# Kernel optimization log

Measured on AMD Instinct MI355X. Metric: run time of the kernel, lower is better.

## Reference

```python
import jax, jax.numpy as jnp
import numpy as np

B, SQ, SK, H, NH = 2, 2048, 2048, 2048, 16
HD = H // NH  # 128
NEG = -1e9


def setup_inputs() -> dict:
    key = jax.random.key(0)
    ks = jax.random.split(key, 8)
    hidden_states = jax.random.normal(ks[0], (B, SQ, H), dtype=jnp.float32)
    # key already transposed/expanded for baddbmm: [B*nh, head_dim, key_len]
    k = jax.random.normal(ks[1], (B * NH, HD, SK), dtype=jnp.float32)
    v = jax.random.normal(ks[2], (B, NH, SK, HD), dtype=jnp.float32)
    # additive float causal mask [B, 1, Sq, Sk]
    causal = jnp.tril(jnp.ones((SQ, SK), dtype=bool))
    attention_mask = jnp.where(causal, 0.0, NEG).astype(jnp.float32)
    attention_mask = jnp.broadcast_to(attention_mask[None, None], (B, 1, SQ, SK))
    w_q = jax.random.normal(ks[3], (H, H), dtype=jnp.float32) * 0.02
    b_q = jnp.zeros((H,), dtype=jnp.float32)
    w_proj = jax.random.normal(ks[4], (H, H), dtype=jnp.float32) * 0.02
    b_proj = jnp.zeros((H,), dtype=jnp.float32)
    return {
        "hidden_states": hidden_states,
        "key": k,
        "value": v,
        "attention_mask": attention_mask,
        "w_q": w_q,
        "b_q": b_q,
        "w_proj": w_proj,
        "b_proj": b_proj,
    }


def reference(hidden_states, key, value, attention_mask, w_q, b_q, w_proj, b_proj):
    dtype = hidden_states.dtype
    scale = 1.0 / (HD ** 0.5)  # scale_attn_weights=True, attention_multiplier=None
    # q projection: [B, Sq, H] -> [B, nh, Sq, hd]
    q = hidden_states @ w_q.T + b_q
    q = q.reshape(B, SQ, NH, HD).transpose(0, 2, 1, 3)
    # key comes in as [B*nh, hd, Sk]
    k = key.reshape(B, NH, HD, SK)
    # scores = mask + scale * q @ k  (baddbmm with beta=1)
    scores = attention_mask + scale * jnp.einsum("bhqd,bhdk->bhqk", q, k)
    # softmax in fp32 (attention_softmax_in_fp32=True), cast back
    probs = jax.nn.softmax(scores.astype(jnp.float32), axis=-1).astype(dtype)
    # attn_pdrop=0 -> no dropout
    out = jnp.einsum("bhqk,bhkd->bhqd", probs, value)  # [B, nh, Sq, hd]
    out = out.transpose(0, 2, 1, 3).reshape(B, SQ, H)
    out = out @ w_proj.T + b_proj  # resid_pdrop=0 -> no dropout
    return out
```

## Files before the change

### kernel.cpp

```cpp
#include <hip/hip_runtime.h>
#include <hip/hip_bf16.h>

typedef __bf16 bf16;
typedef __bf16 bf16x4 __attribute__((ext_vector_type(4)));
typedef __bf16 bf16x8 __attribute__((ext_vector_type(8)));
typedef float  f32x4  __attribute__((ext_vector_type(4)));
typedef unsigned int u32;

#define B_   2
#define SQ_  2048
#define SK_  2048
#define H_   2048
#define NH_  16
#define HD_  128
#define BH_  (B_*NH_)

__device__ inline void gl_lds16(const bf16* g, bf16* l) {
  __builtin_amdgcn_global_load_lds(
      (const __attribute__((address_space(1))) u32*)(const void*)g,
      (__attribute__((address_space(3))) u32*)(void*)l,
      16, 0, 0);
}

__device__ inline float exp2_fast(float x) {
  float r; asm("v_exp_f32 %0, %1" : "=v"(r) : "v"(x)); return r;
}

__global__ __launch_bounds__(256) void cvt_f32_bf16(const float* __restrict__ in,
                                                    bf16* __restrict__ out, int n4) {
  int i = blockIdx.x * blockDim.x + threadIdx.x;
  int stride = gridDim.x * blockDim.x;
  for (; i < n4; i += stride) {
    float4 v = ((const float4*)in)[i];
    bf16x4 w; w[0] = (bf16)v.x; w[1] = (bf16)v.y; w[2] = (bf16)v.z; w[3] = (bf16)v.w;
    ((bf16x4*)out)[i] = w;
  }
}

__global__ __launch_bounds__(256) void transpose_cvt(const float* __restrict__ in,
                                                     bf16* __restrict__ out, int R, int C) {
  __shared__ float tile[64][65];
  const int bh = blockIdx.z;
  const int r0 = blockIdx.y * 64, c0 = blockIdx.x * 64;
  const float* src = in + (size_t)bh * R * C;
  bf16* dst = out + (size_t)bh * R * C;
  const int t = threadIdx.x;
  const int tx = t & 15, ty = t >> 4;
#pragma unroll
  for (int p = 0; p < 4; ++p) {
    int rr = ty + p * 16;
    float4 v = *(const float4*)&src[(size_t)(r0 + rr) * C + c0 + tx * 4];
    tile[rr][tx * 4 + 0] = v.x; tile[rr][tx * 4 + 1] = v.y;
    tile[rr][tx * 4 + 2] = v.z; tile[rr][tx * 4 + 3] = v.w;
  }
  __syncthreads();
#pragma unroll
  for (int p = 0; p < 4; ++p) {
    int cc = ty + p * 16;
    bf16x4 w;
#pragma unroll
    for (int i = 0; i < 4; ++i) w[i] = (bf16)tile[tx * 4 + i][cc];
    *(bf16x4*)&dst[(size_t)(c0 + cc) * R + r0 + tx * 4] = w;
  }
}

template <typename OutT>
__global__ __launch_bounds__(256) void gemm_bt(const bf16* __restrict__ A,
                                               const bf16* __restrict__ Bw,
                                               const float* __restrict__ bias,
                                               OutT* __restrict__ C,
                                               int M, int N, int K, float osc) {
  __shared__ bf16 Abuf[128 * 32];
  __shared__ bf16 Bbuf[128 * 32];
  const int nbn = N >> 7;
  int wg = blockIdx.x, nwg = gridDim.x;
  int swz = (nwg & 7) ? wg : ((wg & 7) * (nwg >> 3) + (wg >> 3));
  int bm = swz / nbn, bn = swz % nbn;
  const int t = threadIdx.x, lane = t & 63, wid = t >> 6;
  const int r = lane & 15, g = lane >> 4;
  const int wr = wid >> 1, wc = wid & 1;
  const size_t m0 = (size_t)bm * 128, n0 = (size_t)bn * 128;

  f32x4 acc[4][4];
#pragma unroll
  for (int m = 0; m < 4; ++m)
#pragma unroll
    for (int n = 0; n < 4; ++n) acc[m][n] = (f32x4){0.f, 0.f, 0.f, 0.f};

  for (int k0 = 0; k0 < K; k0 += 32) {
    __syncthreads();
#pragma unroll
    for (int p = 0; p < 2; ++p) {
      int c = p * 256 + t;
      int row = c >> 2, off = c & 3;
      gl_lds16(A + (m0 + row) * K + k0 + off * 8, &Abuf[(p * 256 + wid * 64) * 8]);
      gl_lds16(Bw + (n0 + row) * K + k0 + off * 8, &Bbuf[(p * 256 + wid * 64) * 8]);
    }
    __syncthreads();
    bf16x8 af[4], bfr[4];
#pragma unroll
    for (int m = 0; m < 4; ++m)
      af[m] = *(const bf16x8*)&Abuf[(wr * 64 + m * 16 + r) * 32 + g * 8];
#pragma unroll
    for (int n = 0; n < 4; ++n)
      bfr[n] = *(const bf16x8*)&Bbuf[(wc * 64 + n * 16 + r) * 32 + g * 8];
#pragma unroll
    for (int m = 0; m < 4; ++m)
#pragma unroll
      for (int n = 0; n < 4; ++n)
        acc[m][n] = __builtin_amdgcn_mfma_f32_16x16x32_bf16(af[m], bfr[n], acc[m][n], 0, 0, 0);
  }

  float bv[4];
#pragma unroll
  for (int n = 0; n < 4; ++n) bv[n] = bias[n0 + wc * 64 + n * 16 + r];
#pragma unroll
  for (int m = 0; m < 4; ++m)
#pragma unroll
    for (int n = 0; n < 4; ++n)
#pragma unroll
      for (int rr = 0; rr < 4; ++rr) {
        size_t row = m0 + wr * 64 + m * 16 + g * 4 + rr;
        size_t col = n0 + wc * 64 + n * 16 + r;
        C[row * N + col] = (OutT)((acc[m][n][rr] + bv[n]) * osc);
      }
}

__device__ __forceinline__ void softmax_prep(const f32x4 (&s)[4], bool diag,
                                             int r, int g, int qbase,
                                             float (&mrun)[4], float (&lpart)[4],
                                             f32x4 (&acc)[8], bf16* pldsw,
                                             bf16x8 (&pa)[2]) {
  float sv[4][4];
#pragma unroll
  for (int sb = 0; sb < 4; ++sb)
#pragma unroll
    for (int rr = 0; rr < 4; ++rr) {
      float x = s[sb][rr];
      if (diag && (sb * 16 + r > qbase + g * 4 + rr)) x = -3.0e38f;
      sv[sb][rr] = x;
    }
  float pm[4];
  bool cond = true;
#pragma unroll
  for (int rr = 0; rr < 4; ++rr) {
    pm[rr] = fmaxf(fmaxf(sv[0][rr], sv[1][rr]), fmaxf(sv[2][rr], sv[3][rr]));
    cond = cond && (pm[rr] <= mrun[rr] + 10.0f);
  }
  if (!__all(cond ? 1 : 0)) {
    f32x4 corrv;
#pragma unroll
    for (int rr = 0; rr < 4; ++rr) {
      float mx = pm[rr];
#pragma unroll
      for (int d = 1; d < 16; d <<= 1) mx = fmaxf(mx, __shfl_xor(mx, d));
      float mnew = fmaxf(mrun[rr], mx);
      float corr = exp2_fast(mrun[rr] - mnew);
      mrun[rr] = mnew;
      lpart[rr] *= corr;
      corrv[rr] = corr;
    }
#pragma unroll
    for (int nb = 0; nb < 8; ++nb) acc[nb] *= corrv;
  }
#pragma unroll
  for (int sb = 0; sb < 4; ++sb)
#pragma unroll
    for (int rr = 0; rr < 4; ++rr) {
      float p = exp2_fast(sv[sb][rr] - mrun[rr]);
      lpart[rr] += p;
      pldsw[(g * 4 + rr) * 68 + sb * 16 + r] = (bf16)p;
    }
#pragma unroll
  for (int k2 = 0; k2 < 2; ++k2)
    pa[k2] = *(const bf16x8*)&pldsw[r * 68 + k2 * 32 + g * 8];
}

__global__ __launch_bounds__(256, 2) void flash_attn(const bf16* __restrict__ Q,
                                                     const bf16* __restrict__ Kt,
                                                     const bf16* __restrict__ Vt,
                                                     bf16* __restrict__ O) {
  __shared__ bf16 Klds[2][64 * 128];
  __shared__ bf16 Vlds[2][128 * 64];
  __shared__ bf16 Plds[4][16 * 68];

  const int id = blockIdx.x;
  const int pr = (id >> 3) & 15;
  const int bh = (id & 7) + 8 * (id >> 7);
  const int qtA = 31 - pr, qtB = pr;
  const int b = bh >> 4, h = bh & 15;
  const int t = threadIdx.x, lane = t & 63, wid = t >> 6;
  const int r = lane & 15, g = lane >> 4;

  const bf16* Kbase = Kt + (size_t)bh * SK_ * HD_;
  const bf16* Vbase = Vt + (size_t)bh * HD_ * SK_;
  bf16* pldsw = &Plds[wid][0];

  size_t kSrc[4], vSrc[4];
#pragma unroll
  for (int p = 0; p < 4; ++p) {
    int c = p * 256 + t;
    { int row = c >> 4, off = c & 15, src = off ^ (row & 7);
      kSrc[p] = (size_t)row * HD_ + src * 8; }
    { int row = c >> 3, off = c & 7, src = off ^ (row & 7);
      vSrc[p] = (size_t)row * SK_ + src * 8; }
  }

  const size_t qrowA = ((size_t)(b * SQ_ + qtA * 64 + wid * 16 + r)) * H_ + (size_t)h * HD_;
  const size_t qrowB = ((size_t)(b * SQ_ + qtB * 64 + wid * 16 + r)) * H_ + (size_t)h * HD_;
  bf16x8 qfA[4], qfB[4];
#pragma unroll
  for (int kk = 0; kk < 4; ++kk) {
    qfA[kk] = *(const bf16x8*)&Q[qrowA + kk * 32 + g * 8];
    qfB[kk] = *(const bf16x8*)&Q[qrowB + kk * 32 + g * 8];
  }

  f32x4 accA[8], accB[8];
  float mrunA[4], lpartA[4], mrunB[4], lpartB[4];
#pragma unroll
  for (int i = 0; i < 8; ++i) { accA[i] = (f32x4){0.f,0.f,0.f,0.f}; accB[i] = (f32x4){0.f,0.f,0.f,0.f}; }
#pragma unroll
  for (int i = 0; i < 4; ++i) { mrunA[i] = -3.0e38f; lpartA[i] = 0.f; mrunB[i] = -3.0e38f; lpartB[i] = 0.f; }

  int cur = 0;
#pragma unroll
  for (int p = 0; p < 4; ++p) {
    gl_lds16(Kbase + kSrc[p], &Klds[cur][(p * 256 + wid * 64) * 8]);
    gl_lds16(Vbase + vSrc[p], &Vlds[cur][(p * 256 + wid * 64) * 8]);
  }
  asm volatile("s_waitcnt vmcnt(0)" ::: "memory");
  __syncthreads();

#pragma unroll 1
  for (int st = 0; st <= qtA; ++st) {
    if (st < qtA) {
      const size_t ks = (size_t)(st + 1) * 64 * HD_;
      const size_t vs = (size_t)(st + 1) * 64;
#pragma unroll
      for (int p = 0; p < 4; ++p) {
        gl_lds16(Kbase + ks + kSrc[p], &Klds[cur ^ 1][(p * 256 + wid * 64) * 8]);
        gl_lds16(Vbase + vs + vSrc[p], &Vlds[cur ^ 1][(p * 256 + wid * 64) * 8]);
      }
    }
    const bool both = (st <= qtB);

    f32x4 sA[4], sB[4];
#pragma unroll
    for (int sb = 0; sb < 4; ++sb) { sA[sb] = (f32x4){0.f,0.f,0.f,0.f}; sB[sb] = (f32x4){0.f,0.f,0.f,0.f}; }
    __builtin_amdgcn_s_setprio(1);
    if (both) {
#pragma unroll
      for (int sb = 0; sb < 4; ++sb) {
        const int srow = sb * 16 + r;
#pragma unroll
        for (int kk = 0; kk < 4; ++kk) {
          bf16x8 kf = *(const bf16x8*)&Klds[cur][srow * 128 + (((kk * 4 + g) ^ (srow & 7)) * 8)];
          sA[sb] = __builtin_amdgcn_mfma_f32_16x16x32_bf16(qfA[kk], kf, sA[sb], 0, 0, 0);
          sB[sb] = __builtin_amdgcn_mfma_f32_16x16x32_bf16(qfB[kk], kf, sB[sb], 0, 0, 0);
        }
      }
    } else {
#pragma unroll
      for (int sb = 0; sb < 4; ++sb) {
        const int srow = sb * 16 + r;
#pragma unroll
        for (int kk = 0; kk < 4; ++kk) {
          bf16x8 kf = *(const bf16x8*)&Klds[cur][srow * 128 + (((kk * 4 + g) ^ (srow & 7)) * 8)];
          sA[sb] = __builtin_amdgcn_mfma_f32_16x16x32_bf16(qfA[kk], kf, sA[sb], 0, 0, 0);
        }
      }
    }
    __builtin_amdgcn_s_setprio(0);

    bf16x8 paA[2], paB[2];
    softmax_prep(sA, st == qtA, r, g, wid * 16, mrunA, lpartA, accA, pldsw, paA);
    if (both) softmax_prep(sB, st == qtB, r, g, wid * 16, mrunB, lpartB, accB, pldsw, paB);

    __builtin_amdgcn_s_setprio(1);
    if (both) {
#pragma unroll
      for (int nb = 0; nb < 8; ++nb) {
        const int drow = nb * 16 + r;
#pragma unroll
        for (int k2 = 0; k2 < 2; ++k2) {
          bf16x8 vf = *(const bf16x8*)&Vlds[cur][drow * 64 + (((k2 * 4 + g) ^ (drow & 7)) * 8)];
          accA[nb] = __builtin_amdgcn_mfma_f32_16x16x32_bf16(paA[k2], vf, accA[nb], 0, 0, 0);
          accB[nb] = __builtin_amdgcn_mfma_f32_16x16x32_bf16(paB[k2], vf, accB[nb], 0, 0, 0);
        }
      }
    } else {
#pragma unroll
      for (int nb = 0; nb < 8; ++nb) {
        const int drow = nb * 16 + r;
#pragma unroll
        for (int k2 = 0; k2 < 2; ++k2) {
          bf16x8 vf = *(const bf16x8*)&Vlds[cur][drow * 64 + (((k2 * 4 + g) ^ (drow & 7)) * 8)];
          accA[nb] = __builtin_amdgcn_mfma_f32_16x16x32_bf16(paA[k2], vf, accA[nb], 0, 0, 0);
        }
      }
    }
    __builtin_amdgcn_s_setprio(0);

    asm volatile("s_waitcnt vmcnt(0)" ::: "memory");
    __syncthreads();
    cur ^= 1;
  }

  float invA[4], invB[4];
#pragma unroll
  for (int rr = 0; rr < 4; ++rr) {
    float la = lpartA[rr], lb = lpartB[rr];
#pragma unroll
    for (int d = 1; d < 16; d <<= 1) { la += __shfl_xor(la, d); lb += __shfl_xor(lb, d); }
    invA[rr] = 1.0f / la; invB[rr] = 1.0f / lb;
  }
#pragma unroll
  for (int nb = 0; nb < 8; ++nb)
#pragma unroll
    for (int rr = 0; rr < 4; ++rr) {
      size_t rowA = (size_t)(b * SQ_ + qtA * 64 + wid * 16 + g * 4 + rr);
      size_t rowB = (size_t)(b * SQ_ + qtB * 64 + wid * 16 + g * 4 + rr);
      O[rowA * H_ + (size_t)h * HD_ + nb * 16 + r] = (bf16)(accA[nb][rr] * invA[rr]);
      O[rowB * H_ + (size_t)h * HD_ + nb * 16 + r] = (bf16)(accB[nb][rr] * invB[rr]);
    }
}

extern "C" void kernel_launch(void* const* d_in, const int* in_sizes, int n_in,
                              void* d_out, int out_size, void* d_ws, size_t ws_size,
                              hipStream_t stream) {
  const float* hidden = (const float*)d_in[0];
  const float* key    = (const float*)d_in[1];
  const float* value  = (const float*)d_in[2];
  const float* w_q    = (const float*)d_in[4];
  const float* b_q    = (const float*)d_in[5];
  const float* w_proj = (const float*)d_in[6];
  const float* b_proj = (const float*)d_in[7];
  float* out = (float*)d_out;

  const size_t N_HID = (size_t)B_ * SQ_ * H_;
  const size_t N_W   = (size_t)H_ * H_;
  const size_t N_KV  = (size_t)BH_ * SK_ * HD_;
  const float SC2 = 0.08838834764831845f * 1.4426950408889634f;

  bf16* hid_bf  = (bf16*)d_ws;
  bf16* wq_bf   = hid_bf + N_HID;
  bf16* wp_bf   = wq_bf + N_W;
  bf16* k_bf    = wp_bf + N_W;
  bf16* vt_bf   = k_bf + N_KV;
  bf16* q_bf    = vt_bf + N_KV;
  bf16* attn_bf = hid_bf;

  cvt_f32_bf16<<<2048, 256, 0, stream>>>(hidden, hid_bf, (int)(N_HID / 4));
  cvt_f32_bf16<<<1024, 256, 0, stream>>>(w_q, wq_bf, (int)(N_W / 4));
  cvt_f32_bf16<<<1024, 256, 0, stream>>>(w_proj, wp_bf, (int)(N_W / 4));
  transpose_cvt<<<dim3(SK_ / 64, HD_ / 64, BH_), 256, 0, stream>>>(key, k_bf, HD_, SK_);
  transpose_cvt<<<dim3(HD_ / 64, SK_ / 64, BH_), 256, 0, stream>>>(value, vt_bf, SK_, HD_);

  gemm_bt<bf16><<<(B_ * SQ_ / 128) * (H_ / 128), 256, 0, stream>>>(
      hid_bf, wq_bf, b_q, q_bf, B_ * SQ_, H_, H_, SC2);

  flash_attn<<<512, 256, 0, stream>>>(q_bf, k_bf, vt_bf, attn_bf);

  gemm_bt<float><<<(B_ * SQ_ / 128) * (H_ / 128), 256, 0, stream>>>(
      attn_bf, wp_bf, b_proj, out, B_ * SQ_, H_, H_, 1.0f);
}
```

Before: 235.1 us.

## Use 128-row query tiles with two sequential passes per flash-attention block

Flash attention now assigns each block two 128-row query tiles (a far tile and a near tile), processed one after the other, with each wave owning 32 query rows as two 16-row fragments. Previously each block interleaved two 64-row tiles. The larger tile lets each K/V tile loaded into shared memory serve twice as many query rows, cutting K/V traffic. The grid halves to 256 blocks and launch bounds drop to one block per SM, which lowers occupancy and may leave CUs underused. Causal masking handles partially active fragments near the diagonal.

After: 249.0 us. 1.06x slower.

```diff
diff --git a/kernel.cpp b/kernel.cpp
--- a/kernel.cpp
+++ b/kernel.cpp
@@ -127,7 +127,7 @@
 }
 
 __device__ __forceinline__ void softmax_prep(const f32x4 (&s)[4], bool diag,
-                                             int r, int g, int qbase,
+                                             int r, int g, int qrow_base, int s_base,
                                              float (&mrun)[4], float (&lpart)[4],
                                              f32x4 (&acc)[8], bf16* pldsw,
                                              bf16x8 (&pa)[2]) {
@@ -137,7 +137,7 @@
 #pragma unroll
     for (int rr = 0; rr < 4; ++rr) {
       float x = s[sb][rr];
-      if (diag && (sb * 16 + r > qbase + g * 4 + rr)) x = -3.0e38f;
+      if (diag && (s_base + sb * 16 + r > qrow_base + g * 4 + rr)) x = -3.0e38f;
       sv[sb][rr] = x;
     }
   float pm[4];
@@ -176,25 +176,24 @@
     pa[k2] = *(const bf16x8*)&pldsw[r * 68 + k2 * 32 + g * 8];
 }
 
-__global__ __launch_bounds__(256, 2) void flash_attn(const bf16* __restrict__ Q,
+__global__ __launch_bounds__(256, 1) void flash_attn(const bf16* __restrict__ Q,
                                                      const bf16* __restrict__ Kt,
                                                      const bf16* __restrict__ Vt,
                                                      bf16* __restrict__ O) {
   __shared__ bf16 Klds[2][64 * 128];
   __shared__ bf16 Vlds[2][128 * 64];
-  __shared__ bf16 Plds[4][16 * 68];
+  __shared__ bf16 Plds[4][2][16 * 68];
 
   const int id = blockIdx.x;
-  const int pr = (id >> 3) & 15;
-  const int bh = (id & 7) + 8 * (id >> 7);
-  const int qtA = 31 - pr, qtB = pr;
+  const int pr = (id >> 3) & 7;
+  const int bh = (id & 7) + 8 * (id >> 6);
+  const int qtA = 15 - pr, qtB = pr;
   const int b = bh >> 4, h = bh & 15;
   const int t = threadIdx.x, lane = t & 63, wid = t >> 6;
   const int r = lane & 15, g = lane >> 4;
 
   const bf16* Kbase = Kt + (size_t)bh * SK_ * HD_;
   const bf16* Vbase = Vt + (size_t)bh * HD_ * SK_;
-  bf16* pldsw = &Plds[wid][0];
 
   size_t kSrc[4], vSrc[4];
 #pragma unroll
@@ -206,123 +205,143 @@
       vSrc[p] = (size_t)row * SK_ + src * 8; }
   }
 
-  const size_t qrowA = ((size_t)(b * SQ_ + qtA * 64 + wid * 16 + r)) * H_ + (size_t)h * HD_;
-  const size_t qrowB = ((size_t)(b * SQ_ + qtB * 64 + wid * 16 + r)) * H_ + (size_t)h * HD_;
-  bf16x8 qfA[4], qfB[4];
-#pragma unroll
-  for (int kk = 0; kk < 4; ++kk) {
-    qfA[kk] = *(const bf16x8*)&Q[qrowA + kk * 32 + g * 8];
-    qfB[kk] = *(const bf16x8*)&Q[qrowB + kk * 32 + g * 8];
-  }
-
-  f32x4 accA[8], accB[8];
-  float mrunA[4], lpartA[4], mrunB[4], lpartB[4];
-#pragma unroll
-  for (int i = 0; i < 8; ++i) { accA[i] = (f32x4){0.f,0.f,0.f,0.f}; accB[i] = (f32x4){0.f,0.f,0.f,0.f}; }
-#pragma unroll
-  for (int i = 0; i < 4; ++i) { mrunA[i] = -3.0e38f; lpartA[i] = 0.f; mrunB[i] = -3.0e38f; lpartB[i] = 0.f; }
-
   int cur = 0;
-#pragma unroll
-  for (int p = 0; p < 4; ++p) {
-    gl_lds16(Kbase + kSrc[p], &Klds[cur][(p * 256 + wid * 64) * 8]);
-    gl_lds16(Vbase + vSrc[p], &Vlds[cur][(p * 256 + wid * 64) * 8]);
-  }
-  asm volatile("s_waitcnt vmcnt(0)" ::: "memory");
-  __syncthreads();
-
 #pragma unroll 1
-  for (int st = 0; st <= qtA; ++st) {
-    if (st < qtA) {
-      const size_t ks = (size_t)(st + 1) * 64 * HD_;
-      const size_t vs = (size_t)(st + 1) * 64;
-#pragma unroll
-      for (int p = 0; p < 4; ++p) {
-        gl_lds16(Kbase + ks + kSrc[p], &Klds[cur ^ 1][(p * 256 + wid * 64) * 8]);
-        gl_lds16(Vbase + vs + vSrc[p], &Vlds[cur ^ 1][(p * 256 + wid * 64) * 8]);
-      }
-    }
-    const bool both = (st <= qtB);
-
-    f32x4 sA[4], sB[4];
-#pragma unroll
-    for (int sb = 0; sb < 4; ++sb) { sA[sb] = (f32x4){0.f,0.f,0.f,0.f}; sB[sb] = (f32x4){0.f,0.f,0.f,0.f}; }
-    __builtin_amdgcn_s_setprio(1);
-    if (both) {
-#pragma unroll
-      for (int sb = 0; sb < 4; ++sb) {
-        const int srow = sb * 16 + r;
-#pragma unroll
-        for (int kk = 0; kk < 4; ++kk) {
-          bf16x8 kf = *(const bf16x8*)&Klds[cur][srow * 128 + (((kk * 4 + g) ^ (srow & 7)) * 8)];
-          sA[sb] = __builtin_amdgcn_mfma_f32_16x16x32_bf16(qfA[kk], kf, sA[sb], 0, 0, 0);
-          sB[sb] = __builtin_amdgcn_mfma_f32_16x16x32_bf16(qfB[kk], kf, sB[sb], 0, 0, 0);
+  for (int pass = 0; pass < 2; ++pass) {
+    const int qt = pass ? qtB : qtA;
+    const int nst = 2 * qt + 2;
+    const int wb = qt * 128 + wid * 32;
+
+    bf16x8 qf[2][4];
+#pragma unroll
+    for (int m = 0; m < 2; ++m) {
+      const size_t qrow = ((size_t)(b * SQ_ + wb + m * 16 + r)) * H_ + (size_t)h * HD_;
+#pragma unroll
+      for (int kk = 0; kk < 4; ++kk)
+        qf[m][kk] = *(const bf16x8*)&Q[qrow + kk * 32 + g * 8];
+    }
+
+    f32x4 acc[2][8];
+    float mrun[2][4], lpart[2][4];
+#pragma unroll
+    for (int m = 0; m < 2; ++m) {
+#pragma unroll
+      for (int i = 0; i < 8; ++i) acc[m][i] = (f32x4){0.f, 0.f, 0.f, 0.f};
+#pragma unroll
+      for (int i = 0; i < 4; ++i) { mrun[m][i] = -3.0e38f; lpart[m][i] = 0.f; }
+    }
+
+#pragma unroll
+    for (int p = 0; p < 4; ++p) {
+      gl_lds16(Kbase + kSrc[p], &Klds[cur][(p * 256 + wid * 64) * 8]);
+      gl_lds16(Vbase + vSrc[p], &Vlds[cur][(p * 256 + wid * 64) * 8]);
+    }
+    asm volatile("s_waitcnt vmcnt(0)" ::: "memory");
+    __syncthreads();
+
+#pragma unroll 1
+    for (int st = 0; st < nst; ++st) {
+      if (st + 1 < nst) {
+        const size_t ks = (size_t)(st + 1) * 64 * HD_;
+        const size_t vs = (size_t)(st + 1) * 64;
+#pragma unroll
+        for (int p = 0; p < 4; ++p) {
+          gl_lds16(Kbase + ks + kSrc[p], &Klds[cur ^ 1][(p * 256 + wid * 64) * 8]);
+          gl_lds16(Vbase + vs + vSrc[p], &Vlds[cur ^ 1][(p * 256 + wid * 64) * 8]);
         }
       }
-    } else {
-#pragma unroll
-      for (int sb = 0; sb < 4; ++sb) {
-        const int srow = sb * 16 + r;
-#pragma unroll
-        for (int kk = 0; kk < 4; ++kk) {
-          bf16x8 kf = *(const bf16x8*)&Klds[cur][srow * 128 + (((kk * 4 + g) ^ (srow & 7)) * 8)];
-          sA[sb] = __builtin_amdgcn_mfma_f32_16x16x32_bf16(qfA[kk], kf, sA[sb], 0, 0, 0);
+      const int sb0 = st * 64;
+      const bool act1 = (sb0 <= wb + 31);
+      const bool act0 = (sb0 <= wb + 15);
+
+      if (act1) {
+        f32x4 sA[2][4];
+#pragma unroll
+        for (int m = 0; m < 2; ++m)
+#pragma unroll
+          for (int sb = 0; sb < 4; ++sb) sA[m][sb] = (f32x4){0.f, 0.f, 0.f, 0.f};
+        __builtin_amdgcn_s_setprio(1);
+        if (act0) {
+#pragma unroll
+          for (int sb = 0; sb < 4; ++sb) {
+            const int srow = sb * 16 + r;
+#pragma unroll
+            for (int kk = 0; kk < 4; ++kk) {
+              bf16x8 kf = *(const bf16x8*)&Klds[cur][srow * 128 + (((kk * 4 + g) ^ (srow & 7)) * 8)];
+              sA[0][sb] = __builtin_amdgcn_mfma_f32_16x16x32_bf16(qf[0][kk], kf, sA[0][sb], 0, 0, 0);
+              sA[1][sb] = __builtin_amdgcn_mfma_f32_16x16x32_bf16(qf[1][kk], kf, sA[1][sb], 0, 0, 0);
+            }
+          }
+        } else {
+#pragma unroll
+          for (int sb = 0; sb < 4; ++sb) {
+            const int srow = sb * 16 + r;
+#pragma unroll
+            for (int kk = 0; kk < 4; ++kk) {
+              bf16x8 kf = *(const bf16x8*)&Klds[cur][srow * 128 + (((kk * 4 + g) ^ (srow & 7)) * 8)];
+              sA[1][sb] = __builtin_amdgcn_mfma_f32_16x16x32_bf16(qf[1][kk], kf, sA[1][sb], 0, 0, 0);
+            }
+          }
         }
+        __builtin_amdgcn_s_setprio(0);
+
+        bf16x8 paf[2][2];
+        if (act0)
+          softmax_prep(sA[0], sb0 + 63 > wb, r, g, wb, sb0,
+                       mrun[0], lpart[0], acc[0], &Plds[wid][0][0], paf[0]);
+        softmax_prep(sA[1], sb0 + 63 > wb + 16, r, g, wb + 16, sb0,
+                     mrun[1], lpart[1], acc[1], &Plds[wid][1][0], paf[1]);
+
+        __builtin_amdgcn_s_setprio(1);
+        if (act0) {
+#pragma unroll
+          for (int nb = 0; nb < 8; ++nb) {
+            const int drow = nb * 16 + r;
+#pragma unroll
+            for (int k2 = 0; k2 < 2; ++k2) {
+              bf16x8 vf = *(const bf16x8*)&Vlds[cur][drow * 64 + (((k2 * 4 + g) ^ (drow & 7)) * 8)];
+              acc[0][nb] = __builtin_amdgcn_mfma_f32_16x16x32_bf16(paf[0][k2], vf, acc[0][nb], 0, 0, 0);
+              acc[1][nb] = __builtin_amdgcn_mfma_f32_16x16x32_bf16(paf[1][k2], vf, acc[1][nb], 0, 0, 0);
+            }
+          }
+        } else {
+#pragma unroll
+          for (int nb = 0; nb < 8; ++nb) {
+            const int drow = nb * 16 + r;
+#pragma unroll
+            for (int k2 = 0; k2 < 2; ++k2) {
+              bf16x8 vf = *(const bf16x8*)&Vlds[cur][drow * 64 + (((k2 * 4 + g) ^ (drow & 7)) * 8)];
+              acc[1][nb] = __builtin_amdgcn_mfma_f32_16x16x32_bf16(paf[1][k2], vf, acc[1][nb], 0, 0, 0);
+            }
+          }
+        }
+        __builtin_amdgcn_s_setprio(0);
       }
-    }
-    __builtin_amdgcn_s_setprio(0);
-
-    bf16x8 paA[2], paB[2];
-    softmax_prep(sA, st == qtA, r, g, wid * 16, mrunA, lpartA, accA, pldsw, paA);
-    if (both) softmax_prep(sB, st == qtB, r, g, wid * 16, mrunB, lpartB, accB, pldsw, paB);
-
-    __builtin_amdgcn_s_setprio(1);
-    if (both) {
-#pragma unroll
-      for (int nb = 0; nb < 8; ++nb) {
-        const int drow = nb * 16 + r;
-#pragma unroll
-        for (int k2 = 0; k2 < 2; ++k2) {
-          bf16x8 vf = *(const bf16x8*)&Vlds[cur][drow * 64 + (((k2 * 4 + g) ^ (drow & 7)) * 8)];
-          accA[nb] = __builtin_amdgcn_mfma_f32_16x16x32_bf16(paA[k2], vf, accA[nb], 0, 0, 0);
-          accB[nb] = __builtin_amdgcn_mfma_f32_16x16x32_bf16(paB[k2], vf, accB[nb], 0, 0, 0);
+
+      asm volatile("s_waitcnt vmcnt(0)" ::: "memory");
+      __syncthreads();
+      cur ^= 1;
+    }
+
+#pragma unroll
+    for (int m = 0; m < 2; ++m) {
+      float inv[4];
+#pragma unroll
+      for (int rr = 0; rr < 4; ++rr) {
+        float la = lpart[m][rr];
+#pragma unroll
+        for (int d = 1; d < 16; d <<= 1) la += __shfl_xor(la, d);
+        inv[rr] = 1.0f / la;
+      }
+#pragma unroll
+      for (int nb = 0; nb < 8; ++nb)
+#pragma unroll
+        for (int rr = 0; rr < 4; ++rr) {
+          size_t row = (size_t)(b * SQ_ + wb + m * 16 + g * 4 + rr);
+          O[row * H_ + (size_t)h * HD_ + nb * 16 + r] = (bf16)(acc[m][nb][rr] * inv[rr]);
         }
-      }
-    } else {
-#pragma unroll
-      for (int nb = 0; nb < 8; ++nb) {
-        const int drow = nb * 16 + r;
-#pragma unroll
-        for (int k2 = 0; k2 < 2; ++k2) {
-          bf16x8 vf = *(const bf16x8*)&Vlds[cur][drow * 64 + (((k2 * 4 + g) ^ (drow & 7)) * 8)];
-          accA[nb] = __builtin_amdgcn_mfma_f32_16x16x32_bf16(paA[k2], vf, accA[nb], 0, 0, 0);
-        }
-      }
-    }
-    __builtin_amdgcn_s_setprio(0);
-
-    asm volatile("s_waitcnt vmcnt(0)" ::: "memory");
-    __syncthreads();
-    cur ^= 1;
-  }
-
-  float invA[4], invB[4];
-#pragma unroll
-  for (int rr = 0; rr < 4; ++rr) {
-    float la = lpartA[rr], lb = lpartB[rr];
-#pragma unroll
-    for (int d = 1; d < 16; d <<= 1) { la += __shfl_xor(la, d); lb += __shfl_xor(lb, d); }
-    invA[rr] = 1.0f / la; invB[rr] = 1.0f / lb;
-  }
-#pragma unroll
-  for (int nb = 0; nb < 8; ++nb)
-#pragma unroll
-    for (int rr = 0; rr < 4; ++rr) {
-      size_t rowA = (size_t)(b * SQ_ + qtA * 64 + wid * 16 + g * 4 + rr);
-      size_t rowB = (size_t)(b * SQ_ + qtB * 64 + wid * 16 + g * 4 + rr);
-      O[rowA * H_ + (size_t)h * HD_ + nb * 16 + r] = (bf16)(accA[nb][rr] * invA[rr]);
-      O[rowB * H_ + (size_t)h * HD_ + nb * 16 + r] = (bf16)(accB[nb][rr] * invB[rr]);
-    }
+    }
+  }
 }
 
 extern "C" void kernel_launch(void* const* d_in, const int* in_sizes, int n_in,
@@ -359,7 +378,7 @@
   gemm_bt<bf16><<<(B_ * SQ_ / 128) * (H_ / 128), 256, 0, stream>>>(
       hid_bf, wq_bf, b_q, q_bf, B_ * SQ_, H_, H_, SC2);
 
-  flash_attn<<<512, 256, 0, stream>>>(q_bf, k_bf, vt_bf, attn_bf);
+  flash_attn<<<256, 256, 0, stream>>>(q_bf, k_bf, vt_bf, attn_bf);
 
   gemm_bt<float><<<(B_ * SQ_ / 128) * (H_ / 128), 256, 0, stream>>>(
       attn_bf, wp_bf, b_proj, out, B_ * SQ_, H_, H_, 1.0f);
```
